# Optimization experiments

Hardware: AMD Instinct MI355X
Metric: run time of the kernel (lower is better)

Reference implementation:

```python
import jax, jax.numpy as jnp
import numpy as np

EMBED_DIM = 1024
NUM_HEADS = 16
HEAD_DIM = EMBED_DIM // NUM_HEADS
SCALE = float(np.sqrt(HEAD_DIM))


def setup_inputs() -> dict:
    key = jax.random.key(0)
    ks = jax.random.split(key, 5)
    B, S, D = 4, 2048, EMBED_DIM
    lim_qkv = 1.0 / np.sqrt(D)
    lim_out = 1.0 / np.sqrt(D)
    return {
        "x": jax.random.normal(ks[0], (B, S, D), dtype=jnp.float32),
        "qkv_w": jax.random.uniform(ks[1], (3 * D, D), jnp.float32, -lim_qkv, lim_qkv),
        "qkv_b": jax.random.uniform(ks[2], (3 * D,), jnp.float32, -lim_qkv, lim_qkv),
        "out_w": jax.random.uniform(ks[3], (D, D), jnp.float32, -lim_out, lim_out),
        "out_b": jax.random.uniform(ks[4], (D,), jnp.float32, -lim_out, lim_out),
    }


def reference(x, qkv_w, qkv_b, out_w, out_b):
    B, S, D = x.shape
    H, Hd = NUM_HEADS, HEAD_DIM
    # qkv projection (torch Linear: x @ W.T + b)
    qkv = x @ qkv_w.T + qkv_b                      # [B, S, 3D]
    qkv = qkv.reshape(B, S, 3, H, Hd)
    q = jnp.transpose(qkv[:, :, 0], (0, 2, 1, 3))  # [B, H, S, Hd]
    k = jnp.transpose(qkv[:, :, 1], (0, 2, 1, 3))
    v = jnp.transpose(qkv[:, :, 2], (0, 2, 1, 3))
    attn = jnp.einsum("bhqd,bhkd->bhqk", q, k) / SCALE  # [B, H, S, S]
    attn = jax.nn.softmax(attn, axis=-1)
    out = jnp.einsum("bhqk,bhkd->bhqd", attn, v)        # [B, H, S, Hd]
    out = jnp.transpose(out, (0, 2, 1, 3)).reshape(B, S, D)
    return out @ out_w.T + out_b
```

## Files before the change

kernel.cpp:

```cpp
#include <hip/hip_runtime.h>

typedef unsigned short u16;
typedef __bf16 bf16x8 __attribute__((ext_vector_type(8)));
typedef __bf16 bf16x4 __attribute__((ext_vector_type(4)));
typedef float f32x4 __attribute__((ext_vector_type(4)));
typedef float f32x16 __attribute__((ext_vector_type(16)));
typedef unsigned u32x2 __attribute__((ext_vector_type(2)));

#define AS1 __attribute__((address_space(1)))
#define AS3 __attribute__((address_space(3)))

__device__ __forceinline__ void gload_lds16(const void* g, void* l) {
  __builtin_amdgcn_global_load_lds((const AS1 void*)g, (AS3 void*)l, 16, 0, 0);
}

__device__ __forceinline__ f32x4 mfma16(bf16x8 a, bf16x8 b, f32x4 c) {
  return __builtin_amdgcn_mfma_f32_16x16x32_bf16(a, b, c, 0, 0, 0);
}
__device__ __forceinline__ f32x16 mfma32(bf16x8 a, bf16x8 b, f32x16 c) {
  return __builtin_amdgcn_mfma_f32_32x32x16_bf16(a, b, c, 0, 0, 0);
}

#define QSCALE 0.18033688011112042f

__global__ __launch_bounds__(256) void k_cvt3(const float* __restrict__ s0, u16* __restrict__ d0, int n0,
                                              const float* __restrict__ s1, u16* __restrict__ d1, int n1,
                                              const float* __restrict__ s2, u16* __restrict__ d2, int n2) {
  int g = (blockIdx.x * 256 + threadIdx.x) * 8;
  const float* src;
  u16* dst;
  int i;
  if (g < n0) { src = s0; dst = d0; i = g; }
  else if (g < n0 + n1) { src = s1; dst = d1; i = g - n0; }
  else if (g < n0 + n1 + n2) { src = s2; dst = d2; i = g - n0 - n1; }
  else return;
  float4 a = *(const float4*)(src + i);
  float4 b = *(const float4*)(src + i + 4);
  union { bf16x8 v; uint4 q; } o;
  o.v[0] = (__bf16)a.x; o.v[1] = (__bf16)a.y; o.v[2] = (__bf16)a.z; o.v[3] = (__bf16)a.w;
  o.v[4] = (__bf16)b.x; o.v[5] = (__bf16)b.y; o.v[6] = (__bf16)b.z; o.v[7] = (__bf16)b.w;
  *(uint4*)(dst + i) = o.q;
}

template <int MODE, int BXN>
__global__ __launch_bounds__(512, 2) void k_gemm_big(
    const u16* __restrict__ A, const u16* __restrict__ W,
    const float* __restrict__ bias, float* __restrict__ Cout,
    u16* __restrict__ Qo, u16* __restrict__ Ko, u16* __restrict__ Vo) {
  __shared__ __align__(16) u16 LDS[3][6 * 4096];

  const int t = threadIdx.x;
  const int lane = t & 63;
  const int w = t >> 6;
  const int wm = w >> 1;
  const int wn = w & 1;
  const int lr = lane & 15;
  const int hi = lane >> 4;

  const int TOT = BXN * 32;
  const int flat = blockIdx.x;
  const int nb = (flat & 7) * (TOT >> 3) + (flat >> 3);
  const int by = nb / BXN;
  const int bx = nb - by * BXN;
  const int m0 = by * 256;
  const int n0 = bx * 128;

  const int tt = t & 255;
  const int g = t >> 8;
  const int tu = (tt & 15) ^ (tt >> 4);
  const int sro = (tu >> 3) * 32 + (tt >> 4);
  const int scol = (tu & 7) * 8;

  auto STAGE = [&](int buf, int kt, int pLo, int pHi) {
    for (int p = pLo; p < pHi; ++p) {
      int st = p * 2 + g;
      const u16* base = (st < 4) ? (A + (size_t)(m0 + st * 64) * 1024)
                                 : (W + (size_t)(n0 + (st - 4) * 64) * 1024);
#pragma unroll
      for (int i = 0; i < 2; ++i)
        gload_lds16(base + (size_t)(sro + i * 16) * 1024 + kt * 64 + scol,
                    &LDS[buf][st * 4096 + i * 2048 + tt * 8]);
    }
  };

  f32x4 acc[4][4] = {};

  STAGE(0, 0, 0, 3);
  STAGE(1, 1, 0, 3);

  for (int kt = 0; kt < 16; ++kt) {
    const int cur = kt % 3;
    const int nxt = (kt + 2) % 3;
    if (kt < 15) asm volatile("s_waitcnt vmcnt(6)" ::: "memory");
    else         asm volatile("s_waitcnt vmcnt(0)" ::: "memory");
    __builtin_amdgcn_sched_barrier(0);
    __builtin_amdgcn_s_barrier();
    __builtin_amdgcn_sched_barrier(0);

    const u16* ab = &LDS[cur][wm * 4096];
    const u16* bb = &LDS[cur][(4 + wn) * 4096];

#pragma unroll
    for (int ks = 0; ks < 2; ++ks) {
      bf16x8 af[4], bfr[4];
#pragma unroll
      for (int mi = 0; mi < 4; ++mi)
        af[mi] = *(const bf16x8*)(ab + ((mi & 1) * 16 + lr) * 128 +
                                  (((ks * 4 + hi + 8 * (mi >> 1)) ^ lr) << 3));
#pragma unroll
      for (int ni = 0; ni < 4; ++ni)
        bfr[ni] = *(const bf16x8*)(bb + ((ni & 1) * 16 + lr) * 128 +
                                   (((ks * 4 + hi + 8 * (ni >> 1)) ^ lr) << 3));
      if (kt + 2 < 16) STAGE(nxt, kt + 2, ks ? 2 : 0, ks ? 3 : 2);
      asm volatile("s_waitcnt lgkmcnt(0)" ::: "memory");
      __builtin_amdgcn_sched_barrier(0);
      __builtin_amdgcn_s_setprio(1);
#pragma unroll
      for (int mi = 0; mi < 4; ++mi)
#pragma unroll
        for (int ni = 0; ni < 4; ++ni)
          acc[mi][ni] = mfma16(bfr[ni], af[mi], acc[mi][ni]);
      __builtin_amdgcn_s_setprio(0);
      __builtin_amdgcn_sched_barrier(0);
      if (ks == 0) __builtin_amdgcn_s_barrier();
    }
  }

  f32x4 bv[4];
#pragma unroll
  for (int ni = 0; ni < 4; ++ni)
    bv[ni] = *(const f32x4*)(bias + n0 + wn * 64 + ni * 16 + hi * 4);

  if (MODE == 0) {
    const int N = BXN * 128;
#pragma unroll
    for (int mi = 0; mi < 4; ++mi) {
      const int m = m0 + wm * 64 + mi * 16 + lr;
#pragma unroll
      for (int ni = 0; ni < 4; ++ni) {
        f32x4 o = acc[mi][ni] + bv[ni];
        *(f32x4*)(Cout + (size_t)m * N + n0 + wn * 64 + ni * 16 + hi * 4) = o;
      }
    }
  } else {
    const int bb16 = m0 >> 11;
    const int sb = (m0 & 2047) + wm * 64;
    const int which = n0 >> 10;
    const int h = ((n0 & 1023) >> 6) + wn;

    if (which < 2) {
      const float scl = (which == 0) ? QSCALE : 1.0f;
      u16* dst = ((which == 0) ? Qo : Ko) + ((size_t)(bb16 * 16 + h) * 2048) * 64;
#pragma unroll
      for (int mi = 0; mi < 4; ++mi) {
        const int s = sb + mi * 16 + lr;
#pragma unroll
        for (int ni = 0; ni < 4; ++ni) {
          bf16x4 pk;
#pragma unroll
          for (int j = 0; j < 4; ++j)
            pk[j] = (__bf16)((acc[mi][ni][j] + bv[ni][j]) * scl);
          *(bf16x4*)(dst + (size_t)s * 64 + ni * 16 + hi * 4) = pk;
        }
      }
    } else {
      __syncthreads();
      u16* scr = &LDS[0][0] + w * 4608;
#pragma unroll
      for (int mi = 0; mi < 4; ++mi)
#pragma unroll
        for (int ni = 0; ni < 4; ++ni)
#pragma unroll
          for (int j = 0; j < 4; ++j) {
            union { __bf16 b; u16 u; } cv;
            cv.b = (__bf16)(acc[mi][ni][j] + bv[ni][j]);
            scr[(ni * 16 + hi * 4 + j) * 72 + mi * 16 + lr] = cv.u;
          }
      asm volatile("s_waitcnt lgkmcnt(0)" ::: "memory");
      __builtin_amdgcn_sched_barrier(0);
      u16* dst = Vo + ((size_t)((bb16 * 16 + h) * 64 + lane)) * 2048 + sb;
#pragma unroll
      for (int mc = 0; mc < 8; ++mc) {
        bf16x8 vv = *(const bf16x8*)(scr + lane * 72 + mc * 8);
        *(bf16x8*)(dst + mc * 8) = vv;
      }
    }
  }
}

__global__ __launch_bounds__(256, 4) void k_attn(const u16* __restrict__ Q,
                                                 const u16* __restrict__ K,
                                                 const u16* __restrict__ Vt,
                                                 u16* __restrict__ ctx) {
  __shared__ __align__(16) u16 Ks[2][64 * 64];
  __shared__ __align__(16) u16 Vs[2][64 * 64];

  const int t = threadIdx.x;
  const int lane = t & 63;
  const int w = t >> 6;
  const int r31 = lane & 31;
  const int hw = lane >> 5;

  const int bid = blockIdx.x;
  const int nb = (bid & 7) * 128 + (bid >> 3);
  const int bh = nb >> 4;
  const int q0 = (nb & 15) * 128;

  const u16* qp = Q + (size_t)bh * 2048 * 64;
  const u16* kp = K + (size_t)bh * 2048 * 64;
  const u16* vp = Vt + (size_t)bh * 64 * 2048;

  const int tu = (t & 15) ^ (t >> 4);
  const int srow = (tu >> 3) * 32 + (t >> 4);
  const int scol = (tu & 7) * 8;

#pragma unroll
  for (int i = 0; i < 2; i++)
    gload_lds16(kp + (size_t)(srow + i * 16) * 64 + scol, Ks[0] + i * 2048 + t * 8);
#pragma unroll
  for (int i = 0; i < 2; i++)
    gload_lds16(vp + (size_t)(srow + i * 16) * 2048 + scol, Vs[0] + i * 2048 + t * 8);

  bf16x8 aq[4];
  const u16* qrow = qp + (size_t)(q0 + w * 32 + r31) * 64 + hw * 8;
#pragma unroll
  for (int kd = 0; kd < 4; kd++) aq[kd] = *(const bf16x8*)(qrow + kd * 16);

  bf16x8 ones;
#pragma unroll
  for (int e = 0; e < 8; e++) ones[e] = (__bf16)1.0f;
  const f32x16 Z = {};

  f32x16 o0 = {}, o1 = {}, l_acc = {};

  for (int it = 0; it < 32; it++) {
    const int cur = it & 1;
    asm volatile("s_waitcnt vmcnt(0)" ::: "memory");
    __builtin_amdgcn_sched_barrier(0);
    __builtin_amdgcn_s_barrier();
    __builtin_amdgcn_sched_barrier(0);

    if (it + 1 < 32) {
      const int ktn = (it + 1) * 64;
      u16* kd_ = Ks[cur ^ 1];
      u16* vd_ = Vs[cur ^ 1];
#pragma unroll
      for (int i = 0; i < 2; i++)
        gload_lds16(kp + (size_t)(ktn + srow + i * 16) * 64 + scol,
                    kd_ + i * 2048 + t * 8);
#pragma unroll
      for (int i = 0; i < 2; i++)
        gload_lds16(vp + (size_t)(srow + i * 16) * 2048 + ktn + scol,
                    vd_ + i * 2048 + t * 8);
    }

    const u16* kb = Ks[cur];
    const u16* vb = Vs[cur];

    __builtin_amdgcn_s_setprio(1);
    f32x16 s0, s1;
    {
      bf16x8 ka0 = *(const bf16x8*)(kb + r31 * 128 + (((hw) ^ (r31 & 15)) << 3));
      bf16x8 ka1 = *(const bf16x8*)(kb + r31 * 128 + (((8 + hw) ^ (r31 & 15)) << 3));
      s0 = mfma32(ka0, aq[0], Z);
      s1 = mfma32(ka1, aq[0], Z);
    }
#pragma unroll
    for (int kd = 1; kd < 4; kd++) {
      int sl0 = (((kd * 2 + hw) ^ (r31 & 15)) << 3);
      int sl1 = (((8 + kd * 2 + hw) ^ (r31 & 15)) << 3);
      bf16x8 ka0 = *(const bf16x8*)(kb + r31 * 128 + sl0);
      bf16x8 ka1 = *(const bf16x8*)(kb + r31 * 128 + sl1);
      s0 = mfma32(ka0, aq[kd], s0);
      s1 = mfma32(ka1, aq[kd], s1);
    }
    __builtin_amdgcn_s_setprio(0);

#pragma unroll
    for (int e = 0; e < 16; e++) {
      s0[e] = __builtin_amdgcn_exp2f(s0[e]);
      s1[e] = __builtin_amdgcn_exp2f(s1[e]);
    }

    __builtin_amdgcn_s_setprio(1);
#pragma unroll
    for (int tile = 0; tile < 2; tile++) {
      f32x16 st = tile ? s1 : s0;
      unsigned pk[8];
#pragma unroll
      for (int p = 0; p < 8; p++) {
        union { __bf16 h[2]; unsigned u; } cv;
        cv.h[0] = (__bf16)st[2 * p];
        cv.h[1] = (__bf16)st[2 * p + 1];
        pk[p] = cv.u;
      }
#pragma unroll
      for (int c = 0; c < 2; c++) {
        u32x2 ra = __builtin_amdgcn_permlane32_swap(pk[4 * c], pk[4 * c + 2], false, false);
        u32x2 rb = __builtin_amdgcn_permlane32_swap(pk[4 * c + 1], pk[4 * c + 3], false, false);
        union { unsigned u[4]; bf16x8 v; } pf;
        pf.u[0] = ra[0]; pf.u[1] = rb[0]; pf.u[2] = ra[1]; pf.u[3] = rb[1];
        const int kap = tile * 2 + c;
        int slv0 = (((kap * 2 + hw) ^ (r31 & 15)) << 3);
        int slv1 = (((8 + kap * 2 + hw) ^ (r31 & 15)) << 3);
        bf16x8 v0 = *(const bf16x8*)(vb + r31 * 128 + slv0);
        bf16x8 v1 = *(const bf16x8*)(vb + r31 * 128 + slv1);
        o0 = mfma32(v0, pf.v, o0);
        o1 = mfma32(v1, pf.v, o1);
        l_acc = mfma32(ones, pf.v, l_acc);
      }
    }
    __builtin_amdgcn_s_setprio(0);
  }

  const int bb = bh >> 4, h = bh & 15;
  const float inv = 1.0f / l_acc[0];
  const size_t base = (size_t)(bb * 2048 + q0 + w * 32 + r31) * 1024 + h * 64;
#pragma unroll
  for (int g = 0; g < 4; g++) {
    bf16x4 p0, p1;
#pragma unroll
    for (int j = 0; j < 4; j++) {
      p0[j] = (__bf16)(o0[g * 4 + j] * inv);
      p1[j] = (__bf16)(o1[g * 4 + j] * inv);
    }
    *(bf16x4*)(ctx + base + g * 8 + hw * 4) = p0;
    *(bf16x4*)(ctx + base + 32 + g * 8 + hw * 4) = p1;
  }
}

extern "C" void kernel_launch(void* const* d_in, const int* in_sizes, int n_in,
                              void* d_out, int out_size, void* d_ws, size_t ws_size,
                              hipStream_t stream) {
  const float* x = (const float*)d_in[0];
  const float* qkv_w = (const float*)d_in[1];
  const float* qkv_b = (const float*)d_in[2];
  const float* out_w = (const float*)d_in[3];
  const float* out_b = (const float*)d_in[4];
  float* out = (float*)d_out;
  char* ws = (char*)d_ws;

  u16* xb    = (u16*)(ws + 0);
  u16* wqkvb = (u16*)(ws + 16777216);
  u16* wob   = (u16*)(ws + 23068672);
  u16* Qb    = (u16*)(ws + 25165824);
  u16* Kb    = (u16*)(ws + 41943040);
  u16* Vtb   = (u16*)(ws + 58720256);
  u16* ctx   = xb;

  k_cvt3<<<6144, 256, 0, stream>>>(x, xb, 8388608,
                                   qkv_w, wqkvb, 3145728,
                                   out_w, wob, 1048576);

  k_gemm_big<1, 24><<<768, 512, 0, stream>>>(xb, wqkvb, qkv_b, nullptr,
                                             Qb, Kb, Vtb);
  k_attn<<<1024, 256, 0, stream>>>(Qb, Kb, Vtb, ctx);
  k_gemm_big<0, 8><<<256, 512, 0, stream>>>(ctx, wob, out_b, out,
                                            nullptr, nullptr, nullptr);
}
```

Before: 195.7 us.

## Add dedicated 128x128-tile output projection GEMM kernel with more blocks

Replaces the generic big-tile GEMM used for the output projection (256 blocks of 512 threads) with a new kernel using 128x128 output tiles, 256 threads and 512 blocks. It double-buffers A and W tiles in LDS through direct global-to-LDS loads, splitting each prefetch across the two k-substeps. The aim is better occupancy and load balance across the CUs for the 8192x1024x1024 GEMM. In exchange each tile reuses less data, so global and L2 traffic goes up.

```diff
diff --git a/kernel.cpp b/kernel.cpp
--- a/kernel.cpp
+++ b/kernel.cpp
@@ -188,6 +188,97 @@
   }
 }
 
+__global__ __launch_bounds__(256, 2) void k_out128(
+    const u16* __restrict__ A, const u16* __restrict__ W,
+    const float* __restrict__ bias, float* __restrict__ Cout) {
+  __shared__ __align__(16) u16 LDS[2][4 * 4096];
+
+  const int t = threadIdx.x;
+  const int lane = t & 63;
+  const int w = t >> 6;
+  const int wm = w >> 1;
+  const int wn = w & 1;
+  const int lr = lane & 15;
+  const int hi = lane >> 4;
+
+  const int flat = blockIdx.x;
+  const int nb = (flat & 7) * 64 + (flat >> 3);
+  const int by = nb >> 3;
+  const int bx = nb & 7;
+  const int m0 = by * 128;
+  const int n0 = bx * 128;
+
+  const int tu = (t & 15) ^ (t >> 4);
+  const int sro = (tu >> 3) * 32 + (t >> 4);
+  const int scol = (tu & 7) * 8;
+
+  auto STAGE = [&](int buf, int kt, int pLo, int pHi) {
+    for (int p = pLo; p < pHi; ++p) {
+      const u16* base = (p < 2) ? (A + (size_t)(m0 + p * 64) * 1024)
+                                : (W + (size_t)(n0 + (p - 2) * 64) * 1024);
+#pragma unroll
+      for (int i = 0; i < 2; ++i)
+        gload_lds16(base + (size_t)(sro + i * 16) * 1024 + kt * 64 + scol,
+                    &LDS[buf][p * 4096 + i * 2048 + t * 8]);
+    }
+  };
+
+  f32x4 acc[4][4] = {};
+
+  STAGE(0, 0, 0, 4);
+
+  for (int kt = 0; kt < 16; ++kt) {
+    const int cur = kt & 1;
+    asm volatile("s_waitcnt vmcnt(0)" ::: "memory");
+    __builtin_amdgcn_sched_barrier(0);
+    __builtin_amdgcn_s_barrier();
+    __builtin_amdgcn_sched_barrier(0);
+
+    const u16* ab = &LDS[cur][wm * 4096];
+    const u16* bb = &LDS[cur][(2 + wn) * 4096];
+
+#pragma unroll
+    for (int ks = 0; ks < 2; ++ks) {
+      bf16x8 af[4], bfr[4];
+#pragma unroll
+      for (int mi = 0; mi < 4; ++mi)
+        af[mi] = *(const bf16x8*)(ab + ((mi & 1) * 16 + lr) * 128 +
+                                  (((ks * 4 + hi + 8 * (mi >> 1)) ^ lr) << 3));
+#pragma unroll
+      for (int ni = 0; ni < 4; ++ni)
+        bfr[ni] = *(const bf16x8*)(bb + ((ni & 1) * 16 + lr) * 128 +
+                                   (((ks * 4 + hi + 8 * (ni >> 1)) ^ lr) << 3));
+      if (kt + 1 < 16) STAGE(cur ^ 1, kt + 1, ks ? 2 : 0, ks ? 4 : 2);
+      asm volatile("s_waitcnt lgkmcnt(0)" ::: "memory");
+      __builtin_amdgcn_sched_barrier(0);
+      __builtin_amdgcn_s_setprio(1);
+#pragma unroll
+      for (int mi = 0; mi < 4; ++mi)
+#pragma unroll
+        for (int ni = 0; ni < 4; ++ni)
+          acc[mi][ni] = mfma16(bfr[ni], af[mi], acc[mi][ni]);
+      __builtin_amdgcn_s_setprio(0);
+      __builtin_amdgcn_sched_barrier(0);
+      if (ks == 0) __builtin_amdgcn_s_barrier();
+    }
+  }
+
+  f32x4 bv[4];
+#pragma unroll
+  for (int ni = 0; ni < 4; ++ni)
+    bv[ni] = *(const f32x4*)(bias + n0 + wn * 64 + ni * 16 + hi * 4);
+
+#pragma unroll
+  for (int mi = 0; mi < 4; ++mi) {
+    const int m = m0 + wm * 64 + mi * 16 + lr;
+#pragma unroll
+    for (int ni = 0; ni < 4; ++ni) {
+      f32x4 o = acc[mi][ni] + bv[ni];
+      *(f32x4*)(Cout + (size_t)m * 1024 + n0 + wn * 64 + ni * 16 + hi * 4) = o;
+    }
+  }
+}
+
 __global__ __launch_bounds__(256, 4) void k_attn(const u16* __restrict__ Q,
                                                  const u16* __restrict__ K,
                                                  const u16* __restrict__ Vt,
@@ -355,6 +446,5 @@
   k_gemm_big<1, 24><<<768, 512, 0, stream>>>(xb, wqkvb, qkv_b, nullptr,
                                              Qb, Kb, Vtb);
   k_attn<<<1024, 256, 0, stream>>>(Qb, Kb, Vtb, ctx);
-  k_gemm_big<0, 8><<<256, 512, 0, stream>>>(ctx, wob, out_b, out,
-                                            nullptr, nullptr, nullptr);
-}
+  k_out128<<<512, 256, 0, stream>>>(ctx, wob, out_b, out);
+}
```

Result: no change. 196.0 us (+0.1%).
